# Kernel optimization log

Measured on AMD Instinct MI355X. Metric: run time of the kernel, lower is better.

The kernel has to match this reference:

```python
import jax, jax.numpy as jnp
import numpy as np

BLOCK_M = 64          # Triton BLOCK_M assumed from first autotune config
SPEAKER, SCENE, STAGE = 1, 2, 3
NUM_HEADS, HEAD_SIZE = 12, 64


def setup_inputs() -> dict:
    key = jax.random.key(0)
    ks = jax.random.split(key, 6)
    B, T, E = 4, 1024, 768
    H, D = NUM_HEADS, HEAD_SIZE
    x = jax.random.normal(ks[0], (B, T, E), jnp.float32)
    idx = jax.random.randint(ks[1], (B, T), 0, 32000)
    struct_embed = jax.random.normal(ks[2], (4, E), jnp.float32) * 0.02
    w_qkv = jax.random.normal(ks[3], (3 * H * D, E), jnp.float32) * 0.02
    w_out = jax.random.normal(ks[4], (E, H * D), jnp.float32) * 0.02
    b_out = jnp.zeros((E,), jnp.float32)
    return {"x": x, "idx": idx, "struct_embed": struct_embed,
            "w_qkv": w_qkv, "w_out": w_out, "b_out": b_out}


def _attention(q, k, v):
    # q,k,v: [B,H,T,D]. Faithful to the Triton kernel (eval mode):
    # q/k rounded to bf16, fp32 dot, logit clamp [-30,30], exp clamp 1e5,
    # +1e-10 denom, output rounded to bf16. Query rows with
    # (row % BLOCK_M) % 3 == 0 are zeroed by the kernel's load mask.
    T, D = q.shape[2], q.shape[3]
    keep = ((jnp.arange(T) % BLOCK_M) % 3 != 0).astype(q.dtype)
    qb = q.astype(jnp.bfloat16).astype(jnp.float32) * keep[None, None, :, None]
    kb = k.astype(jnp.bfloat16).astype(jnp.float32)
    scale = 1.0 / np.sqrt(D).astype(np.float32)
    scores = jnp.einsum('bhmd,bhnd->bhmn', qb, kb) * scale
    scores = jnp.clip(scores, -30.0, 30.0)
    m = jnp.max(scores, axis=-1, keepdims=True)
    p = jnp.minimum(jnp.exp(scores - m), 1e5)
    acc = jnp.einsum('bhmn,bhnd->bhmd', p, v)
    out = acc / (jnp.sum(p, axis=-1, keepdims=True) + 1e-10)
    return out.astype(jnp.bfloat16).astype(jnp.float32)


def reference(x, idx, struct_embed, w_qkv, w_out, b_out):
    B, T, E = x.shape
    H, D = NUM_HEADS, HEAD_SIZE
    # structure embedding addition (struct_dropout is identity in eval)
    struct_ids = ((idx == SPEAKER) * 1 + (idx == SCENE) * 2
                  + (idx == STAGE) * 3)
    x = x + struct_embed[struct_ids]
    # fused QKV projection (no bias)
    qkv = x @ w_qkv.T                              # [B,T,3HD]
    q, k, v = jnp.split(qkv, 3, axis=-1)
    q = q.reshape(B, T, H, D).transpose(0, 2, 1, 3)
    k = k.reshape(B, T, H, D).transpose(0, 2, 1, 3)
    v = v.reshape(B, T, H, D).transpose(0, 2, 1, 3)
    attn = _attention(q, k, v)                     # [B,H,T,D]
    attn = attn.transpose(0, 2, 1, 3).reshape(B, T, H * D)
    return attn @ w_out.T + b_out
```

## Files before the change

### kernel.cpp

```cpp
#include <hip/hip_runtime.h>
#include <hip/hip_bf16.h>

typedef __attribute__((ext_vector_type(8))) short bf16x8;
typedef __attribute__((ext_vector_type(4))) short bf16x4;
typedef __attribute__((ext_vector_type(4))) float f32x4;

#define MFMA16(a, b, c) __builtin_amdgcn_mfma_f32_16x16x32_bf16(a, b, c, 0, 0, 0)

__device__ __forceinline__ unsigned short f2bf(float f) {
  unsigned u = __float_as_uint(f);
  u += 0x7fff + ((u >> 16) & 1);
  return (unsigned short)(u >> 16);
}
__device__ __forceinline__ float bf2f(unsigned short s) {
  return __uint_as_float(((unsigned)s) << 16);
}
__device__ __forceinline__ void gload16(const unsigned short* g, unsigned short* l) {
  __builtin_amdgcn_global_load_lds((const __attribute__((address_space(1))) void*)g,
                                   (__attribute__((address_space(3))) void*)l, 16, 0, 0);
}
__device__ __forceinline__ int xcd_swz(int lin, int nwg) {
  int cpx = nwg >> 3;
  return (lin & 7) * cpx + (lin >> 3);
}

__global__ __launch_bounds__(256) void prep_all(const float* __restrict__ x,
                                                const int* __restrict__ idx,
                                                const float* __restrict__ se,
                                                const float* __restrict__ wqkv,
                                                const float* __restrict__ wout,
                                                unsigned short* __restrict__ xb,
                                                unsigned short* __restrict__ wqkvb,
                                                unsigned short* __restrict__ woutb) {
  int bid = blockIdx.x;
  int tid = threadIdx.x;
  if (bid < 3072) {
    int i = bid * 256 + tid;
    int row = i / 192, c4 = i % 192;
    int id = idx[row];
    int sid = (id == 1) ? 1 : (id == 2) ? 2 : (id == 3) ? 3 : 0;
    float4 v = ((const float4*)x)[i];
    float4 s = ((const float4*)se)[sid * 192 + c4];
    ushort4 o;
    o.x = f2bf(v.x + s.x); o.y = f2bf(v.y + s.y);
    o.z = f2bf(v.z + s.z); o.w = f2bf(v.w + s.w);
    *(ushort4*)(xb + (size_t)i * 4) = o;
  } else if (bid < 3072 + 1728) {
    int i = (bid - 3072) * 256 + tid;
    float4 v = ((const float4*)wqkv)[i];
    ushort4 u;
    u.x = f2bf(v.x); u.y = f2bf(v.y); u.z = f2bf(v.z); u.w = f2bf(v.w);
    ((ushort4*)wqkvb)[i] = u;
  } else {
    int i = (bid - 4800) * 256 + tid;
    float4 v = ((const float4*)wout)[i];
    ushort4 u;
    u.x = f2bf(v.x); u.y = f2bf(v.y); u.z = f2bf(v.z); u.w = f2bf(v.w);
    ((ushort4*)woutb)[i] = u;
  }
}

__global__ __launch_bounds__(256) void gemm_qkv(const unsigned short* __restrict__ A,
                                                const unsigned short* __restrict__ B,
                                                unsigned short* __restrict__ Cout,
                                                unsigned short* __restrict__ vT,
                                                int N, int K) {
  __shared__ unsigned short As[2][4096];
  __shared__ unsigned short Bs[2][4096];
  int tid = threadIdx.x;
  int lane = tid & 63, wid = tid >> 6;
  int l15 = lane & 15, lhi = lane >> 4;
  int wr = wid >> 1, wc = wid & 1;
  int gy = gridDim.y;
  int lin = blockIdx.x + gridDim.x * blockIdx.y;
  int swz = xcd_swz(lin, gridDim.x * gy);
  long tm = (long)(swz / gy) * 128;
  long tn = (long)(swz % gy) * 128;
  f32x4 acc[4][4];
  const f32x4 z4 = {0.f, 0.f, 0.f, 0.f};
  for (int i = 0; i < 4; ++i)
    for (int j = 0; j < 4; ++j) acc[i][j] = z4;

  int wbase = tid & ~63;
  int row0 = tid >> 2;
  int kc = (tid & 3) * 8;
  const unsigned short* Ar0 = &A[(tm + row0) * (long)K + kc];
  const unsigned short* Ar1 = &A[(tm + 64 + row0) * (long)K + kc];
  const unsigned short* Br0 = &B[(tn + row0) * (long)K + kc];
  const unsigned short* Br1 = &B[(tn + 64 + row0) * (long)K + kc];

  auto stage = [&](int b, int k0) {
    gload16(Ar0 + k0, &As[b][wbase * 8]);
    gload16(Ar1 + k0, &As[b][2048 + wbase * 8]);
    gload16(Br0 + k0, &Bs[b][wbase * 8]);
    gload16(Br1 + k0, &Bs[b][2048 + wbase * 8]);
  };

  stage(0, 0);
  __syncthreads();
  int buf = 0;
  for (int k0 = 0; k0 < K; k0 += 32) {
    if (k0 + 32 < K) stage(buf ^ 1, k0 + 32);
    bf16x8 af[4], bfr[4];
#pragma unroll
    for (int mi = 0; mi < 4; ++mi)
      af[mi] = *(const bf16x8*)&As[buf][(wr * 64 + mi * 16 + l15) * 32 + lhi * 8];
#pragma unroll
    for (int nj = 0; nj < 4; ++nj)
      bfr[nj] = *(const bf16x8*)&Bs[buf][(wc * 64 + nj * 16 + l15) * 32 + lhi * 8];
#pragma unroll
    for (int mi = 0; mi < 4; ++mi)
#pragma unroll
      for (int nj = 0; nj < 4; ++nj)
        acc[mi][nj] = MFMA16(af[mi], bfr[nj], acc[mi][nj]);
    __syncthreads();
    buf ^= 1;
  }

  if (tn >= 1536) {
    int b = (int)(tm >> 10);
    int hbase = (int)((tn - 1536) >> 6) + wc;
    int tb = (int)(tm & 1023) + wr * 64 + lhi * 4;
#pragma unroll
    for (int nj = 0; nj < 4; ++nj) {
      int dd = nj * 16 + l15;
      size_t vbase = ((size_t)(b * 12 + hbase)) * 65536 + (size_t)dd * 1024;
#pragma unroll
      for (int mi = 0; mi < 4; ++mi) {
        ushort4 o;
        o.x = f2bf(acc[mi][nj][0]); o.y = f2bf(acc[mi][nj][1]);
        o.z = f2bf(acc[mi][nj][2]); o.w = f2bf(acc[mi][nj][3]);
        *(ushort4*)&vT[vbase + tb + mi * 16] = o;
      }
    }
    return;
  }

#pragma unroll
  for (int mi = 0; mi < 4; ++mi) {
    long row = tm + wr * 64 + mi * 16 + lhi * 4;
#pragma unroll
    for (int nj = 0; nj < 4; ++nj) {
      long col = tn + wc * 64 + nj * 16 + l15;
#pragma unroll
      for (int r = 0; r < 4; ++r)
        Cout[(row + r) * (long)N + col] = f2bf(acc[mi][nj][r]);
    }
  }
}

__global__ __launch_bounds__(256) void gemm_out(const unsigned short* __restrict__ A,
                                                const unsigned short* __restrict__ B,
                                                float* __restrict__ Cout,
                                                const float* __restrict__ bias,
                                                int N, int K) {
  __shared__ unsigned short As[2][64 * 32];
  __shared__ unsigned short Bs[2][64 * 32];
  int tid = threadIdx.x;
  int lane = tid & 63, w = tid >> 6;
  int l15 = lane & 15, lhi = lane >> 4;
  int gy = gridDim.y;
  int lin = blockIdx.x + gridDim.x * blockIdx.y;
  int swz = xcd_swz(lin, gridDim.x * gy);
  long tm = (long)(swz / gy) * 64;
  long tn = (long)(swz % gy) * 64;
  f32x4 acc[4];
  const f32x4 z4 = {0.f, 0.f, 0.f, 0.f};
#pragma unroll
  for (int n = 0; n < 4; ++n) acc[n] = z4;

  int wbase8 = (tid & ~63) * 8;
  int row0 = tid >> 2;
  int kc = (tid & 3) * 8;
  const unsigned short* Ar = &A[(tm + row0) * (long)K + kc];
  const unsigned short* Br = &B[(tn + row0) * (long)K + kc];

  auto stage = [&](int b, int k0) {
    gload16(Ar + k0, &As[b][wbase8]);
    gload16(Br + k0, &Bs[b][wbase8]);
  };

  stage(0, 0);
  __syncthreads();
  int buf = 0;
  for (int k0 = 0; k0 < K; k0 += 32) {
    if (k0 + 32 < K) stage(buf ^ 1, k0 + 32);
    bf16x8 af = *(const bf16x8*)&As[buf][(w * 16 + l15) * 32 + lhi * 8];
    bf16x8 bfr[4];
#pragma unroll
    for (int n = 0; n < 4; ++n)
      bfr[n] = *(const bf16x8*)&Bs[buf][(n * 16 + l15) * 32 + lhi * 8];
#pragma unroll
    for (int n = 0; n < 4; ++n)
      acc[n] = MFMA16(af, bfr[n], acc[n]);
    __syncthreads();
    buf ^= 1;
  }

  long row = tm + w * 16 + lhi * 4;
#pragma unroll
  for (int n = 0; n < 4; ++n) {
    long col = tn + n * 16 + l15;
    float bv = bias[col];
#pragma unroll
    for (int r = 0; r < 4; ++r)
      Cout[(row + r) * (long)N + col] = acc[n][r] + bv;
  }
}

__global__ __launch_bounds__(256) void attn_fwd(const unsigned short* __restrict__ qkv,
                                                const unsigned short* __restrict__ vT,
                                                unsigned short* __restrict__ attnb) {
  __shared__ unsigned short Ks[2][4096];
  __shared__ unsigned short Vs[2][4096];
  int tid = threadIdx.x;
  int lane = tid & 63, w = tid >> 6;
  int l15 = lane & 15, lhi = lane >> 4;
  int sw = l15 & 7;
  int lin = blockIdx.x + gridDim.x * blockIdx.y;
  int swz = xcd_swz(lin, 768);
  int qt = swz & 15, bh = swz >> 4;
  int b = bh / 12, h = bh % 12;

  int r8 = lane >> 3;
  int cK = ((lane & 7) ^ r8) << 3;
  int wbase = (tid & ~63) * 8;
  const unsigned short* kg = qkv + (size_t)(b * 1024) * 2304 + 768 + h * 64 + cK;
  const unsigned short* vg = vT + (size_t)bh * 65536 + cK;

#pragma unroll
  for (int p = 0; p < 2; ++p) {
    int row = p * 32 + w * 8 + r8;
    gload16(kg + (size_t)row * 2304, &Ks[0][p * 2048 + wbase]);
    gload16(vg + (size_t)row * 1024, &Vs[0][p * 2048 + wbase]);
  }

  int qrl = w * 16 + l15;
  bf16x8 qf0 = {0, 0, 0, 0, 0, 0, 0, 0}, qf1 = {0, 0, 0, 0, 0, 0, 0, 0};
  if (qrl % 3 != 0) {
    const unsigned short* qp =
        &qkv[(size_t)(b * 1024 + qt * 64 + qrl) * 2304 + h * 64 + lhi * 8];
    qf0 = *(const bf16x8*)qp;
    qf1 = *(const bf16x8*)(qp + 32);
  }

  const f32x4 z4 = {0.f, 0.f, 0.f, 0.f};
  f32x4 acc[4];
#pragma unroll
  for (int dg = 0; dg < 4; ++dg) acc[dg] = z4;
  f32x4 accd = z4;
  const short one_bf = (short)0x3F80;
  const bf16x8 ONES = {one_bf, one_bf, one_bf, one_bf, one_bf, one_bf, one_bf, one_bf};

  __syncthreads();

  int buf = 0;
  for (int t = 0; t < 16; ++t) {
    if (t < 15) {
      size_t k0 = (size_t)(t + 1) * 64;
#pragma unroll
      for (int p = 0; p < 2; ++p) {
        int row = p * 32 + w * 8 + r8;
        gload16(kg + (k0 + row) * 2304, &Ks[buf ^ 1][p * 2048 + wbase]);
        gload16(vg + (size_t)row * 1024 + k0, &Vs[buf ^ 1][p * 2048 + wbase]);
      }
    }
    const unsigned short* ks = Ks[buf];
    const unsigned short* vs = Vs[buf];

    bf16x8 paf[2];
#pragma unroll
    for (int g = 0; g < 4; ++g) {
      const unsigned short* kr = &ks[(g * 16 + l15) * 64];
      bf16x8 kf0 = *(const bf16x8*)&kr[(lhi ^ sw) << 3];
      bf16x8 kf1 = *(const bf16x8*)&kr[((lhi + 4) ^ sw) << 3];
      f32x4 sg = MFMA16(kf0, qf0, z4);
      sg = MFMA16(kf1, qf1, sg);
#pragma unroll
      for (int r = 0; r < 4; ++r) {
        float pv = exp2f(sg[r] * 0.18033688011f);
        paf[g >> 1][(g & 1) * 4 + r] = (short)f2bf(pv);
      }
    }

    __builtin_amdgcn_s_setprio(1);
    accd = MFMA16(paf[0], ONES, accd);
    accd = MFMA16(paf[1], ONES, accd);
#pragma unroll
    for (int dg = 0; dg < 4; ++dg) {
      const unsigned short* vr = &vs[(dg * 16 + l15) * 64];
#pragma unroll
      for (int kh = 0; kh < 2; ++kh) {
        int o0 = kh * 32 + lhi * 4;
        int o1 = o0 + 16;
        bf16x4 v0 = *(const bf16x4*)&vr[(((o0 >> 3) ^ sw) << 3) + (o0 & 7)];
        bf16x4 v1 = *(const bf16x4*)&vr[(((o1 >> 3) ^ sw) << 3) + (o1 & 7)];
        bf16x8 vf = __builtin_shufflevector(v0, v1, 0, 1, 2, 3, 4, 5, 6, 7);
        acc[dg] = MFMA16(paf[kh], vf, acc[dg]);
      }
    }
    __builtin_amdgcn_s_setprio(0);
    __syncthreads();
    buf ^= 1;
  }

#pragma unroll
  for (int r = 0; r < 4; ++r) {
    float inv = 1.f / (accd[r] + 1e-10f);
    int orow = qt * 64 + w * 16 + lhi * 4 + r;
    size_t obase = (size_t)(b * 1024 + orow) * 768 + h * 64;
#pragma unroll
    for (int dg = 0; dg < 4; ++dg)
      attnb[obase + dg * 16 + l15] = f2bf(acc[dg][r] * inv);
  }
}

extern "C" void kernel_launch(void* const* d_in, const int* in_sizes, int n_in,
                              void* d_out, int out_size, void* d_ws, size_t ws_size,
                              hipStream_t stream) {
  (void)in_sizes; (void)n_in; (void)out_size; (void)ws_size;
  const float* x    = (const float*)d_in[0];
  const int*   idx  = (const int*)d_in[1];
  const float* se   = (const float*)d_in[2];
  const float* wqkv = (const float*)d_in[3];
  const float* wout = (const float*)d_in[4];
  const float* bout = (const float*)d_in[5];
  float* out = (float*)d_out;

  char* ws = (char*)d_ws;
  unsigned short* xb    = (unsigned short*)(ws);
  unsigned short* wqkvb = (unsigned short*)(ws + 6291456);
  unsigned short* woutb = (unsigned short*)(ws + 9830400);
  unsigned short* qkvb  = (unsigned short*)(ws + 11010048);
  unsigned short* vT    = (unsigned short*)(ws + 29884416);
  unsigned short* attnb = (unsigned short*)(ws + 36175872);

  prep_all<<<5376, 256, 0, stream>>>(x, idx, se, wqkv, wout, xb, wqkvb, woutb);
  gemm_qkv<<<dim3(32, 18), 256, 0, stream>>>(xb, wqkvb, qkvb, vT, 2304, 768);
  attn_fwd<<<dim3(16, 48), 256, 0, stream>>>(qkvb, vT, attnb);
  gemm_out<<<dim3(64, 12), 256, 0, stream>>>(attnb, woutb, out, bout, 768, 768);
}
```

Before: 86.59 us.

## Triple-buffer K/V tiles in attention with explicit vmcnt waits and single barrier

Moves the attention kernel's K/V shared-memory staging from double to triple buffering, prefetching two tiles ahead. It replaces the end-of-iteration __syncthreads with a partial s_waitcnt vmcnt plus one s_barrier at the top of each iteration, so up to two tile loads can be in flight during compute. It also issues the Q fragment loads before the K/V prefetches. The cost is 50% more LDS per block, which may reduce occupancy, and correctness now depends on hand-counted vmcnt values being right.

```diff
diff --git a/kernel.cpp b/kernel.cpp
--- a/kernel.cpp
+++ b/kernel.cpp
@@ -6,6 +6,8 @@
 typedef __attribute__((ext_vector_type(4))) float f32x4;
 
 #define MFMA16(a, b, c) __builtin_amdgcn_mfma_f32_16x16x32_bf16(a, b, c, 0, 0, 0)
+#define VMCNT4() asm volatile("s_waitcnt vmcnt(4)" ::: "memory")
+#define VMCNT0() asm volatile("s_waitcnt vmcnt(0)" ::: "memory")
 
 __device__ __forceinline__ unsigned short f2bf(float f) {
   unsigned u = __float_as_uint(f);
@@ -211,8 +213,8 @@
 __global__ __launch_bounds__(256) void attn_fwd(const unsigned short* __restrict__ qkv,
                                                 const unsigned short* __restrict__ vT,
                                                 unsigned short* __restrict__ attnb) {
-  __shared__ unsigned short Ks[2][4096];
-  __shared__ unsigned short Vs[2][4096];
+  __shared__ unsigned short Ks[3][4096];
+  __shared__ unsigned short Vs[3][4096];
   int tid = threadIdx.x;
   int lane = tid & 63, w = tid >> 6;
   int l15 = lane & 15, lhi = lane >> 4;
@@ -222,19 +224,6 @@
   int qt = swz & 15, bh = swz >> 4;
   int b = bh / 12, h = bh % 12;
 
-  int r8 = lane >> 3;
-  int cK = ((lane & 7) ^ r8) << 3;
-  int wbase = (tid & ~63) * 8;
-  const unsigned short* kg = qkv + (size_t)(b * 1024) * 2304 + 768 + h * 64 + cK;
-  const unsigned short* vg = vT + (size_t)bh * 65536 + cK;
-
-#pragma unroll
-  for (int p = 0; p < 2; ++p) {
-    int row = p * 32 + w * 8 + r8;
-    gload16(kg + (size_t)row * 2304, &Ks[0][p * 2048 + wbase]);
-    gload16(vg + (size_t)row * 1024, &Vs[0][p * 2048 + wbase]);
-  }
-
   int qrl = w * 16 + l15;
   bf16x8 qf0 = {0, 0, 0, 0, 0, 0, 0, 0}, qf1 = {0, 0, 0, 0, 0, 0, 0, 0};
   if (qrl % 3 != 0) {
@@ -244,6 +233,25 @@
     qf1 = *(const bf16x8*)(qp + 32);
   }
 
+  int r8 = lane >> 3;
+  int cK = ((lane & 7) ^ r8) << 3;
+  int wbase = (tid & ~63) * 8;
+  const unsigned short* kg = qkv + (size_t)(b * 1024) * 2304 + 768 + h * 64 + cK;
+  const unsigned short* vg = vT + (size_t)bh * 65536 + cK;
+
+  auto stage = [&](int bufi, int t) {
+    size_t k0 = (size_t)t * 64;
+#pragma unroll
+    for (int p = 0; p < 2; ++p) {
+      int row = p * 32 + w * 8 + r8;
+      gload16(kg + (k0 + row) * 2304, &Ks[bufi][p * 2048 + wbase]);
+      gload16(vg + (size_t)row * 1024 + k0, &Vs[bufi][p * 2048 + wbase]);
+    }
+  };
+
+  stage(0, 0);
+  stage(1, 1);
+
   const f32x4 z4 = {0.f, 0.f, 0.f, 0.f};
   f32x4 acc[4];
 #pragma unroll
@@ -252,21 +260,13 @@
   const short one_bf = (short)0x3F80;
   const bf16x8 ONES = {one_bf, one_bf, one_bf, one_bf, one_bf, one_bf, one_bf, one_bf};
 
-  __syncthreads();
-
-  int buf = 0;
+  int bc = 0, bp = 2;
   for (int t = 0; t < 16; ++t) {
-    if (t < 15) {
-      size_t k0 = (size_t)(t + 1) * 64;
-#pragma unroll
-      for (int p = 0; p < 2; ++p) {
-        int row = p * 32 + w * 8 + r8;
-        gload16(kg + (k0 + row) * 2304, &Ks[buf ^ 1][p * 2048 + wbase]);
-        gload16(vg + (size_t)row * 1024 + k0, &Vs[buf ^ 1][p * 2048 + wbase]);
-      }
-    }
-    const unsigned short* ks = Ks[buf];
-    const unsigned short* vs = Vs[buf];
+    if (t < 15) VMCNT4(); else VMCNT0();
+    __builtin_amdgcn_s_barrier();
+    if (t + 2 < 16) stage(bp, t + 2);
+    const unsigned short* ks = Ks[bc];
+    const unsigned short* vs = Vs[bc];
 
     bf16x8 paf[2];
 #pragma unroll
@@ -300,8 +300,8 @@
       }
     }
     __builtin_amdgcn_s_setprio(0);
-    __syncthreads();
-    buf ^= 1;
+    bc = (bc == 2) ? 0 : bc + 1;
+    bp = (bp == 2) ? 0 : bp + 1;
   }
 
 #pragma unroll
```

Result: no change. 86.31 us (-0.3%).
